# Performance work log

Hardware: AMD Instinct MI355X
Metric: run time of the kernel (lower is better)

Reference implementation:

```python
import jax, jax.numpy as jnp
import numpy as np

BN_EPS = 1e-5


def setup_inputs() -> dict:
    key = jax.random.key(0)
    ks = jax.random.split(key, 6)
    B, C, N, K, T, O = 8, 64, 4096, 20, 3, 64
    feat = jax.random.normal(ks[0], (B, C, N), dtype=jnp.float32)
    idx = jax.random.randint(ks[1], (B, N, K), 0, N, dtype=jnp.int32)
    group_pc = jax.random.normal(ks[2], (B, 3, N, K), dtype=jnp.float32)
    weights = jax.random.normal(ks[3], (B, 20, T, N, K), dtype=jnp.float32) * 0.05
    conv_w = jax.random.normal(ks[4], (O, C * T, K), dtype=jnp.float32) * 0.02
    gamma = jnp.ones((O,), dtype=jnp.float32)
    beta = jnp.zeros((O,), dtype=jnp.float32)
    return {"feat": feat, "idx": idx, "group_pc": group_pc, "weights": weights,
            "conv_w": conv_w, "gamma": gamma, "beta": beta}


def _poly_terms(group_pc):
    # group_pc: (B, 3, N, K) -> 20 Taylor terms (B, 20, N, K)
    X, Y, Z = group_pc[:, 0], group_pc[:, 1], group_pc[:, 2]
    XX, YY, ZZ = X * X, Y * Y, Z * Z
    XY, XZ, YZ = X * Y, X * Z, Y * Z
    ones = jnp.ones_like(X)
    return jnp.stack([
        ones, X, Y, Z,
        XX, YY, ZZ,
        XX * X, YY * Y, ZZ * Z,
        XY, XZ, YZ,
        X * XY, X * XZ, Y * YZ, Y * XY, Z * XZ, Z * YZ, XY * Z,
    ], axis=1)


def reference(feat, idx, group_pc, weights, conv_w, gamma, beta):
    B, C, N = feat.shape
    K = idx.shape[-1]
    T = weights.shape[2]
    # KNN gather: group_feat[b, c, n, j] = feat[b, c, idx[b, n, j]]  -> (B, C, N, K)
    group_feat = jax.vmap(lambda f, i: f[:, i])(feat, idx)
    # 20 polynomial basis terms of XYZ: (B, 20, N, K)
    terms = _poly_terms(group_pc)
    # taylor[b, t, n, k] = sum_p weights[b, p, t, n, k] * terms[b, p, n, k]
    taylor = jnp.einsum('bptnk,bpnk->btnk', weights, terms)
    # Fused outer-product + [1, K] conv (output width 1, no bias since bn=True):
    # out[b, o, n] = sum_{c, t, k} group_feat[b,c,n,k] * taylor[b,t,n,k] * W[o, c*T+t, k]
    w = conv_w.reshape(conv_w.shape[0], C, T, K)
    out = jnp.einsum('bcnk,btnk,octk->bon', group_feat, taylor, w)
    # BatchNorm (training-mode batch stats over B and N) + ReLU
    mean = jnp.mean(out, axis=(0, 2), keepdims=True)
    var = jnp.var(out, axis=(0, 2), keepdims=True)
    out = gamma[None, :, None] * (out - mean) / jnp.sqrt(var + BN_EPS) + beta[None, :, None]
    return jax.nn.relu(out)
```

## Files before the change

### kernel.cpp

```cpp
#include <hip/hip_runtime.h>
#include <hip/hip_bf16.h>

#define B_ 8
#define C_ 64
#define N_ 4096
#define K_ 20
#define T_ 3
#define O_ 64
#define P_ 20
#define NK_ (N_ * K_)
#define BN_EPS 1e-5f
#define KG 5

#define WS_FEATT 0
#define WS_WT (WS_FEATT + B_ * N_ * C_)
#define WS_RAW (WS_WT + 122880)
#define WS_PART (WS_RAW + B_ * O_ * N_)
#define WS_STATS (WS_PART + 131072)

typedef __attribute__((ext_vector_type(8))) _Float16 half8;
typedef __attribute__((ext_vector_type(2))) _Float16 half2v;
typedef __attribute__((ext_vector_type(2))) __fp16 fp16x2;
typedef __attribute__((ext_vector_type(16))) float f32x16;

union UH8 {
    uint4 u;
    half8 h;
    half2v h2[4];
};
union UH2 {
    unsigned u;
    half2v h;
    fp16x2 f;
};

__device__ inline unsigned cvt_pkrtz_u(float a, float b) {
    UH2 x;
    x.f = __builtin_amdgcn_cvt_pkrtz(a, b);
    return x.u;
}

__global__ void k_transpose_feat(const float* __restrict__ feat, float* __restrict__ featT) {
    __shared__ float t[64][65];
    int bid = blockIdx.x;
    int b = bid & 7;
    int n0 = (bid >> 3) << 6;
    int lx = threadIdx.x & 63, ly = threadIdx.x >> 6;
    const float* fp = feat + b * C_ * N_;
#pragma unroll
    for (int cc = 0; cc < 16; ++cc) {
        int c = ly * 16 + cc;
        t[c][lx] = fp[c * N_ + n0 + lx];
    }
    __syncthreads();
    float* op = featT + (b * N_ + n0) * C_;
#pragma unroll
    for (int u = 0; u < 16; ++u) {
        int n = ly * 16 + u;
        op[n * C_ + lx] = t[lx][n];
    }
}

__global__ void k_pack_w(const float* __restrict__ cw, _Float16* __restrict__ Wh) {
    int e = blockIdx.x * 256 + threadIdx.x;
    int j = e & 7;
    int l = (e >> 3) & 63;
    int frag = e >> 9;
    int oh = frag & 1;
    int cc = (frag >> 1) & 3;
    int kt = frag >> 3;
    int t = kt % 3, k = kt / 3;
    int o = oh * 32 + (l & 31);
    int c = cc * 16 + (l >> 5) * 8 + j;
    Wh[e] = (_Float16)cw[o * (C_ * T_ * K_) + (c * T_ + t) * K_ + k];
}

__global__ __launch_bounds__(512, 4) void k_main(const float* __restrict__ featT,
                                                 const _Float16* __restrict__ Wh,
                                                 const float* __restrict__ weights,
                                                 const float* __restrict__ gpc,
                                                 const int* __restrict__ idx,
                                                 float* __restrict__ raw,
                                                 float* __restrict__ part) {
    __shared__ unsigned short E[2][KG][32][68];
    __shared__ union {
        unsigned tayH[T_][K_][32];
        float out[64][36];
    } su;

    const int bid0 = blockIdx.x;
    const int bid = (bid0 & 7) * 128 + (bid0 >> 3);
    const int b = bid >> 7;
    const int n0 = (bid & 127) << 5;
    const int tid = threadIdx.x;
    const int lane = tid & 63;
    const int wv = tid >> 6;
    const int wc = wv & 3;
    const int wo = wv >> 2;
    const int nl = lane & 31;
    const int kf = lane >> 5;
    const int row = tid >> 4, seg = tid & 15;

    const float* fb = featT + (size_t)b * N_ * C_;

    int idxv[K_];
    {
        const int4* ip4 = (const int4*)(idx + (size_t)(b * N_ + n0 + row) * K_);
#pragma unroll
        for (int q = 0; q < 5; ++q) {
            int4 v = ip4[q];
            idxv[q * 4 + 0] = v.x;
            idxv[q * 4 + 1] = v.y;
            idxv[q * 4 + 2] = v.z;
            idxv[q * 4 + 3] = v.w;
        }
    }

    float4 gA[KG], gB[KG];
#pragma unroll
    for (int kk = 0; kk < KG; ++kk)
        gA[kk] = *(const float4*)(fb + (size_t)idxv[kk] * C_ + seg * 4);

    {
        const float* gpcb = gpc + (size_t)b * 3 * NK_ + n0 * K_;
        const float* wb0 = weights + (size_t)b * P_ * T_ * NK_ + n0 * K_;
        for (int e = tid; e < 32 * K_; e += 512) {
            float X = gpcb[e];
            float Y = gpcb[NK_ + e];
            float Z = gpcb[2 * NK_ + e];
            float XX = X * X, YY = Y * Y, ZZ = Z * Z;
            float XY = X * Y, XZ = X * Z, YZ = Y * Z;
            float terms[20];
            terms[0] = 1.f; terms[1] = X;      terms[2] = Y;       terms[3] = Z;
            terms[4] = XX;  terms[5] = YY;     terms[6] = ZZ;
            terms[7] = XX * X; terms[8] = YY * Y; terms[9] = ZZ * Z;
            terms[10] = XY; terms[11] = XZ;    terms[12] = YZ;
            terms[13] = X * XY;
            terms[14] = X * XZ;
            terms[15] = Y * YZ;
            terms[16] = Y * XY;
            terms[17] = Z * XZ;
            terms[18] = Z * YZ;
            terms[19] = XY * Z;
            float a0 = 0.f, a1 = 0.f, a2 = 0.f;
            const float* wp = wb0 + e;
#pragma unroll
            for (int p = 0; p < P_; ++p) {
                float tp = terms[p];
                a0 += wp[0] * tp;
                a1 += wp[(size_t)NK_] * tp;
                a2 += wp[2 * (size_t)NK_] * tp;
                wp += 3 * (size_t)NK_;
            }
            int n = e / K_, k = e - n * K_;
            su.tayH[0][k][n] = cvt_pkrtz_u(a0, a0);
            su.tayH[1][k][n] = cvt_pkrtz_u(a1, a1);
            su.tayH[2][k][n] = cvt_pkrtz_u(a2, a2);
        }
    }

#pragma unroll
    for (int kk = 0; kk < KG; ++kk) {
        uint2 w;
        w.x = cvt_pkrtz_u(gA[kk].x, gA[kk].y);
        w.y = cvt_pkrtz_u(gA[kk].z, gA[kk].w);
        *(uint2*)&E[0][kk][row][seg * 4] = w;
    }
#pragma unroll
    for (int kk = 0; kk < KG; ++kk)
        gA[kk] = *(const float4*)(fb + (size_t)idxv[KG + kk] * C_ + seg * 4);
    __syncthreads();

    f32x16 acc;
#pragma unroll
    for (int i = 0; i < 16; ++i) acc[i] = 0.f;

#pragma unroll
    for (int p = 0; p < 4; ++p) {
        if (p + 2 < 4) {
#pragma unroll
            for (int kk = 0; kk < KG; ++kk) {
                float4 v = *(const float4*)(fb + (size_t)idxv[(p + 2) * KG + kk] * C_ + seg * 4);
                if (p & 1) gA[kk] = v; else gB[kk] = v;
            }
        }
#pragma unroll
        for (int kk = 0; kk < KG; ++kk) {
            UH8 gv;
            gv.u = *(const uint4*)&E[p & 1][kk][nl][wc * 16 + kf * 8];
            const int k = p * KG + kk;
#pragma unroll
            for (int t = 0; t < 3; ++t) {
                UH8 ar;
                ar.u = *(const uint4*)(Wh +
                                       (size_t)((((k * 3 + t) * 4 + wc) * 2 + wo) * 64 + lane) * 8);
                UH2 tv;
                tv.u = su.tayH[t][k][nl];
                UH8 bv;
#pragma unroll
                for (int i = 0; i < 4; ++i) bv.h2[i] = gv.h2[i] * tv.h;
                acc = __builtin_amdgcn_mfma_f32_32x32x16_f16(ar.h, bv.h, acc, 0, 0, 0);
            }
        }
        if (p + 1 < 4) {
#pragma unroll
            for (int kk = 0; kk < KG; ++kk) {
                float4 v = (p & 1) ? gB[kk] : gA[kk];
                uint2 w;
                w.x = cvt_pkrtz_u(v.x, v.y);
                w.y = cvt_pkrtz_u(v.z, v.w);
                *(uint2*)&E[(p + 1) & 1][kk][row][seg * 4] = w;
            }
        }
        __syncthreads();
    }

#pragma unroll 1
    for (int ww = 0; ww < 4; ++ww) {
        if (wc == ww) {
#pragma unroll
            for (int rr = 0; rr < 16; ++rr) {
                int orow = wo * 32 + (rr & 3) + ((rr >> 2) << 3) + (kf << 2);
                if (ww == 0)
                    su.out[orow][nl] = acc[rr];
                else
                    su.out[orow][nl] += acc[rr];
            }
        }
        __syncthreads();
    }

    {
        int o = tid >> 3, sg = tid & 7;
        float4* dst = (float4*)(raw + ((b * O_ + o) * N_) + n0 + sg * 4);
        const float* srow = &su.out[o][sg * 4];
        *dst = make_float4(srow[0], srow[1], srow[2], srow[3]);
    }
    if (tid < 64) {
        float s1 = 0.f, s2 = 0.f;
#pragma unroll 8
        for (int n = 0; n < 32; ++n) {
            float v = su.out[tid][n];
            s1 += v;
            s2 += v * v;
        }
        part[(bid * 64 + tid) * 2 + 0] = s1;
        part[(bid * 64 + tid) * 2 + 1] = s2;
    }
}

__global__ void k_bnstats(const float* __restrict__ part, const float* __restrict__ gamma,
                          const float* __restrict__ beta, float* __restrict__ stats) {
    int o = blockIdx.x;
    int tid = threadIdx.x;
    __shared__ float s1s[256], s2s[256];
    float s1 = 0.f, s2 = 0.f;
    for (int j = tid; j < 1024; j += 256) {
        s1 += part[(j * 64 + o) * 2 + 0];
        s2 += part[(j * 64 + o) * 2 + 1];
    }
    s1s[tid] = s1;
    s2s[tid] = s2;
    __syncthreads();
    for (int s = 128; s > 0; s >>= 1) {
        if (tid < s) {
            s1s[tid] += s1s[tid + s];
            s2s[tid] += s2s[tid + s];
        }
        __syncthreads();
    }
    if (tid == 0) {
        const float cnt = (float)(B_ * N_);
        float mean = s1s[0] / cnt;
        float var = s2s[0] / cnt - mean * mean;
        float sc = gamma[o] * rsqrtf(var + BN_EPS);
        stats[o * 2 + 0] = sc;
        stats[o * 2 + 1] = beta[o] - mean * sc;
    }
}

__global__ void k_finalize(const float* __restrict__ raw, const float* __restrict__ stats,
                           float* __restrict__ out) {
    int e = (blockIdx.x * 256 + threadIdx.x) * 4;
    int o = (e >> 12) & 63;
    float sc = stats[o * 2 + 0], sh = stats[o * 2 + 1];
    float4 v = *(const float4*)(raw + e);
    v.x = fmaxf(v.x * sc + sh, 0.f);
    v.y = fmaxf(v.y * sc + sh, 0.f);
    v.z = fmaxf(v.z * sc + sh, 0.f);
    v.w = fmaxf(v.w * sc + sh, 0.f);
    *(float4*)(out + e) = v;
}

extern "C" void kernel_launch(void* const* d_in, const int* in_sizes, int n_in,
                              void* d_out, int out_size, void* d_ws, size_t ws_size,
                              hipStream_t stream) {
    const float* feat = (const float*)d_in[0];
    const int* idx = (const int*)d_in[1];
    const float* gpc = (const float*)d_in[2];
    const float* weights = (const float*)d_in[3];
    const float* conv_w = (const float*)d_in[4];
    const float* gamma = (const float*)d_in[5];
    const float* beta = (const float*)d_in[6];
    float* out = (float*)d_out;
    float* ws = (float*)d_ws;

    float* featT = ws + WS_FEATT;
    _Float16* Wh = (_Float16*)(ws + WS_WT);
    float* raw = ws + WS_RAW;
    float* part = ws + WS_PART;
    float* stats = ws + WS_STATS;

    hipLaunchKernelGGL(k_transpose_feat, dim3(512), dim3(256), 0, stream, feat, featT);
    hipLaunchKernelGGL(k_pack_w, dim3((K_ * T_ * C_ * O_) / 256), dim3(256), 0, stream, conv_w,
                       Wh);
    hipLaunchKernelGGL(k_main, dim3(B_ * (N_ / 32)), dim3(512), 0, stream, featT, Wh, weights,
                       gpc, idx, raw, part);
    hipLaunchKernelGGL(k_bnstats, dim3(O_), dim3(256), 0, stream, part, gamma, beta, stats);
    hipLaunchKernelGGL(k_finalize, dim3(B_ * O_ * N_ / 4 / 256), dim3(256), 0, stream, raw, stats,
                       out);
}
```

Measured before the change: 70.67 us.

## Split Taylor weight contraction into a separate streaming kernel before main

```diff
diff --git a/kernel.cpp b/kernel.cpp
--- a/kernel.cpp
+++ b/kernel.cpp
@@ -14,7 +14,8 @@
 
 #define WS_FEATT 0
 #define WS_WT (WS_FEATT + B_ * N_ * C_)
-#define WS_RAW (WS_WT + 122880)
+#define WS_TAY (WS_WT + 122880)
+#define WS_RAW (WS_TAY + B_ * T_ * NK_)
 #define WS_PART (WS_RAW + B_ * O_ * N_)
 #define WS_STATS (WS_PART + 131072)
 
@@ -75,10 +76,49 @@
     Wh[e] = (_Float16)cw[o * (C_ * T_ * K_) + (c * T_ + t) * K_ + k];
 }
 
+__global__ void k_taylor(const float* __restrict__ W5, const float* __restrict__ gpc,
+                         unsigned* __restrict__ tayw) {
+    int bid0 = blockIdx.x;
+    int bid = (bid0 & 7) * 320 + (bid0 >> 3);
+    int tid = bid * 256 + threadIdx.x;
+    int b = tid / NK_;
+    int nk = tid - b * NK_;
+    const float X = gpc[b * 3 * NK_ + nk];
+    const float Y = gpc[b * 3 * NK_ + NK_ + nk];
+    const float Z = gpc[b * 3 * NK_ + 2 * NK_ + nk];
+    float XX = X * X, YY = Y * Y, ZZ = Z * Z;
+    float XY = X * Y, XZ = X * Z, YZ = Y * Z;
+    float terms[20];
+    terms[0] = 1.f; terms[1] = X;      terms[2] = Y;       terms[3] = Z;
+    terms[4] = XX;  terms[5] = YY;     terms[6] = ZZ;
+    terms[7] = XX * X; terms[8] = YY * Y; terms[9] = ZZ * Z;
+    terms[10] = XY; terms[11] = XZ;    terms[12] = YZ;
+    terms[13] = X * XY;
+    terms[14] = X * XZ;
+    terms[15] = Y * YZ;
+    terms[16] = Y * XY;
+    terms[17] = Z * XZ;
+    terms[18] = Z * YZ;
+    terms[19] = XY * Z;
+    float a0 = 0.f, a1 = 0.f, a2 = 0.f;
+    const float* wp = W5 + (size_t)b * P_ * T_ * NK_ + nk;
+#pragma unroll
+    for (int p = 0; p < P_; ++p) {
+        float tp = terms[p];
+        a0 += wp[0] * tp;
+        a1 += wp[(size_t)NK_] * tp;
+        a2 += wp[2 * (size_t)NK_] * tp;
+        wp += 3 * (size_t)NK_;
+    }
+    unsigned* tp = tayw + (size_t)b * 3 * NK_ + nk;
+    tp[0] = cvt_pkrtz_u(a0, a0);
+    tp[NK_] = cvt_pkrtz_u(a1, a1);
+    tp[2 * NK_] = cvt_pkrtz_u(a2, a2);
+}
+
 __global__ __launch_bounds__(512, 4) void k_main(const float* __restrict__ featT,
                                                  const _Float16* __restrict__ Wh,
-                                                 const float* __restrict__ weights,
-                                                 const float* __restrict__ gpc,
+                                                 const unsigned* __restrict__ tayw,
                                                  const int* __restrict__ idx,
                                                  float* __restrict__ raw,
                                                  float* __restrict__ part) {
@@ -122,40 +162,12 @@
         gA[kk] = *(const float4*)(fb + (size_t)idxv[kk] * C_ + seg * 4);
 
     {
-        const float* gpcb = gpc + (size_t)b * 3 * NK_ + n0 * K_;
-        const float* wb0 = weights + (size_t)b * P_ * T_ * NK_ + n0 * K_;
+        const unsigned* tp = tayw + (size_t)b * 3 * NK_ + n0 * K_;
         for (int e = tid; e < 32 * K_; e += 512) {
-            float X = gpcb[e];
-            float Y = gpcb[NK_ + e];
-            float Z = gpcb[2 * NK_ + e];
-            float XX = X * X, YY = Y * Y, ZZ = Z * Z;
-            float XY = X * Y, XZ = X * Z, YZ = Y * Z;
-            float terms[20];
-            terms[0] = 1.f; terms[1] = X;      terms[2] = Y;       terms[3] = Z;
-            terms[4] = XX;  terms[5] = YY;     terms[6] = ZZ;
-            terms[7] = XX * X; terms[8] = YY * Y; terms[9] = ZZ * Z;
-            terms[10] = XY; terms[11] = XZ;    terms[12] = YZ;
-            terms[13] = X * XY;
-            terms[14] = X * XZ;
-            terms[15] = Y * YZ;
-            terms[16] = Y * XY;
-            terms[17] = Z * XZ;
-            terms[18] = Z * YZ;
-            terms[19] = XY * Z;
-            float a0 = 0.f, a1 = 0.f, a2 = 0.f;
-            const float* wp = wb0 + e;
-#pragma unroll
-            for (int p = 0; p < P_; ++p) {
-                float tp = terms[p];
-                a0 += wp[0] * tp;
-                a1 += wp[(size_t)NK_] * tp;
-                a2 += wp[2 * (size_t)NK_] * tp;
-                wp += 3 * (size_t)NK_;
-            }
             int n = e / K_, k = e - n * K_;
-            su.tayH[0][k][n] = cvt_pkrtz_u(a0, a0);
-            su.tayH[1][k][n] = cvt_pkrtz_u(a1, a1);
-            su.tayH[2][k][n] = cvt_pkrtz_u(a2, a2);
+            su.tayH[0][k][n] = tp[e];
+            su.tayH[1][k][n] = tp[NK_ + e];
+            su.tayH[2][k][n] = tp[2 * NK_ + e];
         }
     }
 
@@ -307,6 +319,7 @@
 
     float* featT = ws + WS_FEATT;
     _Float16* Wh = (_Float16*)(ws + WS_WT);
+    unsigned* tayw = (unsigned*)(ws + WS_TAY);
     float* raw = ws + WS_RAW;
     float* part = ws + WS_PART;
     float* stats = ws + WS_STATS;
@@ -314,8 +327,9 @@
     hipLaunchKernelGGL(k_transpose_feat, dim3(512), dim3(256), 0, stream, feat, featT);
     hipLaunchKernelGGL(k_pack_w, dim3((K_ * T_ * C_ * O_) / 256), dim3(256), 0, stream, conv_w,
                        Wh);
-    hipLaunchKernelGGL(k_main, dim3(B_ * (N_ / 32)), dim3(512), 0, stream, featT, Wh, weights,
-                       gpc, idx, raw, part);
+    hipLaunchKernelGGL(k_taylor, dim3(B_ * NK_ / 256), dim3(256), 0, stream, weights, gpc, tayw);
+    hipLaunchKernelGGL(k_main, dim3(B_ * (N_ / 32)), dim3(512), 0, stream, featT, Wh, tayw, idx,
+                       raw, part);
     hipLaunchKernelGGL(k_bnstats, dim3(O_), dim3(256), 0, stream, part, gamma, beta, stats);
     hipLaunchKernelGGL(k_finalize, dim3(B_ * O_ * N_ / 4 / 256), dim3(256), 0, stream, raw, stats,
                        out);
```

Result: slower. 84.35 us (+19.4%).

## Restructure gather pipeline, prefetch per-wave weight fragments, pack indices to 16-bit

Applied to the files above, without the earlier changes.

```diff
diff --git a/kernel.cpp b/kernel.cpp
--- a/kernel.cpp
+++ b/kernel.cpp
@@ -66,12 +66,11 @@
     int j = e & 7;
     int l = (e >> 3) & 63;
     int frag = e >> 9;
-    int oh = frag & 1;
-    int cc = (frag >> 1) & 3;
-    int kt = frag >> 3;
-    int t = kt % 3, k = kt / 3;
-    int o = oh * 32 + (l & 31);
-    int c = cc * 16 + (l >> 5) * 8 + j;
+    int t = frag % 3;
+    int k = (frag / 3) % K_;
+    int wcwo = frag / 60;
+    int o = (wcwo & 1) * 32 + (l & 31);
+    int c = (wcwo >> 1) * 16 + (l >> 5) * 8 + j;
     Wh[e] = (_Float16)cw[o * (C_ * T_ * K_) + (c * T_ + t) * K_ + k];
 }
 
@@ -102,24 +101,24 @@
     const int row = tid >> 4, seg = tid & 15;
 
     const float* fb = featT + (size_t)b * N_ * C_;
-
-    int idxv[K_];
+    const _Float16* WhW = Wh + (size_t)(wc * 2 + wo) * (K_ * T_ * 512);
+
+    unsigned idxp[10];
     {
         const int4* ip4 = (const int4*)(idx + (size_t)(b * N_ + n0 + row) * K_);
 #pragma unroll
         for (int q = 0; q < 5; ++q) {
             int4 v = ip4[q];
-            idxv[q * 4 + 0] = v.x;
-            idxv[q * 4 + 1] = v.y;
-            idxv[q * 4 + 2] = v.z;
-            idxv[q * 4 + 3] = v.w;
-        }
-    }
-
-    float4 gA[KG], gB[KG];
+            idxp[q * 2 + 0] = (unsigned)v.x | ((unsigned)v.y << 16);
+            idxp[q * 2 + 1] = (unsigned)v.z | ((unsigned)v.w << 16);
+        }
+    }
+#define IDXAT(kidx) ((idxp[(kidx) >> 1] >> (((kidx)&1) * 16)) & 0xffffu)
+
+    float4 gA[KG];
 #pragma unroll
     for (int kk = 0; kk < KG; ++kk)
-        gA[kk] = *(const float4*)(fb + (size_t)idxv[kk] * C_ + seg * 4);
+        gA[kk] = *(const float4*)(fb + (size_t)IDXAT(kk) * C_ + seg * 4);
 
     {
         const float* gpcb = gpc + (size_t)b * 3 * NK_ + n0 * K_;
@@ -159,31 +158,32 @@
         }
     }
 
-#pragma unroll
-    for (int kk = 0; kk < KG; ++kk) {
-        uint2 w;
-        w.x = cvt_pkrtz_u(gA[kk].x, gA[kk].y);
-        w.y = cvt_pkrtz_u(gA[kk].z, gA[kk].w);
-        *(uint2*)&E[0][kk][row][seg * 4] = w;
-    }
-#pragma unroll
-    for (int kk = 0; kk < KG; ++kk)
-        gA[kk] = *(const float4*)(fb + (size_t)idxv[KG + kk] * C_ + seg * 4);
-    __syncthreads();
-
     f32x16 acc;
 #pragma unroll
     for (int i = 0; i < 16; ++i) acc[i] = 0.f;
 
 #pragma unroll
     for (int p = 0; p < 4; ++p) {
-        if (p + 2 < 4) {
-#pragma unroll
-            for (int kk = 0; kk < KG; ++kk) {
-                float4 v = *(const float4*)(fb + (size_t)idxv[(p + 2) * KG + kk] * C_ + seg * 4);
-                if (p & 1) gA[kk] = v; else gB[kk] = v;
-            }
-        }
+#pragma unroll
+        for (int kk = 0; kk < KG; ++kk) {
+            uint2 w;
+            w.x = cvt_pkrtz_u(gA[kk].x, gA[kk].y);
+            w.y = cvt_pkrtz_u(gA[kk].z, gA[kk].w);
+            *(uint2*)&E[p & 1][kk][row][seg * 4] = w;
+        }
+        if (p + 1 < 4) {
+#pragma unroll
+            for (int kk = 0; kk < KG; ++kk)
+                gA[kk] = *(const float4*)(fb + (size_t)IDXAT((p + 1) * KG + kk) * C_ + seg * 4);
+        }
+        UH8 ar[KG][3];
+#pragma unroll
+        for (int kk = 0; kk < KG; ++kk)
+#pragma unroll
+            for (int t = 0; t < 3; ++t)
+                ar[kk][t].u =
+                    *(const uint4*)(WhW + (((p * KG + kk) * 3 + t) << 9) + lane * 8);
+        __syncthreads();
 #pragma unroll
         for (int kk = 0; kk < KG; ++kk) {
             UH8 gv;
@@ -191,30 +191,17 @@
             const int k = p * KG + kk;
 #pragma unroll
             for (int t = 0; t < 3; ++t) {
-                UH8 ar;
-                ar.u = *(const uint4*)(Wh +
-                                       (size_t)((((k * 3 + t) * 4 + wc) * 2 + wo) * 64 + lane) * 8);
                 UH2 tv;
                 tv.u = su.tayH[t][k][nl];
                 UH8 bv;
 #pragma unroll
                 for (int i = 0; i < 4; ++i) bv.h2[i] = gv.h2[i] * tv.h;
-                acc = __builtin_amdgcn_mfma_f32_32x32x16_f16(ar.h, bv.h, acc, 0, 0, 0);
+                acc = __builtin_amdgcn_mfma_f32_32x32x16_f16(ar[kk][t].h, bv.h, acc, 0, 0, 0);
             }
         }
-        if (p + 1 < 4) {
-#pragma unroll
-            for (int kk = 0; kk < KG; ++kk) {
-                float4 v = (p & 1) ? gB[kk] : gA[kk];
-                uint2 w;
-                w.x = cvt_pkrtz_u(v.x, v.y);
-                w.y = cvt_pkrtz_u(v.z, v.w);
-                *(uint2*)&E[(p + 1) & 1][kk][row][seg * 4] = w;
-            }
-        }
-        __syncthreads();
-    }
-
+    }
+
+    __syncthreads();
 #pragma unroll 1
     for (int ww = 0; ww < 4; ++ww) {
         if (wc == ww) {
```

Result: slower. 98.84 us (+39.9%).
